# Kernel optimization log

Measured on AMD Instinct MI355X. Metric: run time of the kernel, lower is better.

The kernel has to match this reference:

```python
import jax, jax.numpy as jnp
import numpy as np

B, L, D, H, DK, DV = 2, 2048, 512, 8, 64, 64
EPS_LN = 1e-6


def setup_inputs() -> dict:
    key = jax.random.key(0)
    ks = jax.random.split(key, 14)
    ws = 0.02  # weight init scale
    inp = {}
    for i, n in enumerate(["q_r", "q_i", "k_r", "k_i", "v_r", "v_i"]):
        inp[n] = jax.random.normal(ks[i], (B, L, D), jnp.float32)
    for j, n in enumerate(["wq_r", "wq_i", "wk_r", "wk_i", "wv_r", "wv_i", "fc_r", "fc_i"]):
        inp[n] = jax.random.normal(ks[6 + j], (D, D), jnp.float32) * ws
    # complextorch CVLayerNorm affine: (2,2,D) weight, diag = 1/sqrt(2); complex bias = 0
    c = np.float32(1.0 / np.sqrt(2.0))
    ln_w = jnp.zeros((2, 2, D), jnp.float32).at[0, 0].set(c).at[1, 1].set(c)
    inp["ln_w"] = ln_w
    inp["ln_b_r"] = jnp.zeros((D,), jnp.float32)
    inp["ln_b_i"] = jnp.zeros((D,), jnp.float32)
    return inp


def _cv_layernorm(x, ln_w, ln_b_r, ln_b_i):
    # covariance-whitening complex LayerNorm over last dim (complextorch style)
    xr, xi = jnp.real(x), jnp.imag(x)
    xr = xr - jnp.mean(xr, axis=-1, keepdims=True)
    xi = xi - jnp.mean(xi, axis=-1, keepdims=True)
    vrr = jnp.mean(xr * xr, axis=-1, keepdims=True) + EPS_LN
    vii = jnp.mean(xi * xi, axis=-1, keepdims=True) + EPS_LN
    vri = jnp.mean(xr * xi, axis=-1, keepdims=True)
    s = jnp.sqrt(vrr * vii - vri * vri)
    t = jnp.sqrt(vrr + vii + 2.0 * s)
    inv = 1.0 / (s * t)
    rrr, rii, rri = (vii + s) * inv, (vrr + s) * inv, -vri * inv
    yr = rrr * xr + rri * xi
    yi = rri * xr + rii * xi
    out_r = ln_w[0, 0] * yr + ln_w[0, 1] * yi + ln_b_r
    out_i = ln_w[1, 0] * yr + ln_w[1, 1] * yi + ln_b_i
    return out_r, out_i


def _mha(q_r, q_i, k_r, k_i, v_r, v_i, wq_r, wq_i, wk_r, wk_i, wv_r, wv_i,
         fc_r, fc_i, ln_w, ln_b_r, ln_b_i):
    q = (q_r + 1j * q_i).astype(jnp.complex64)
    k = (k_r + 1j * k_i).astype(jnp.complex64)
    v = (v_r + 1j * v_i).astype(jnp.complex64)
    Wq = (wq_r + 1j * wq_i).astype(jnp.complex64)
    Wk = (wk_r + 1j * wk_i).astype(jnp.complex64)
    Wv = (wv_r + 1j * wv_i).astype(jnp.complex64)
    Wfc = (fc_r + 1j * fc_i).astype(jnp.complex64)
    b, lq = q.shape[0], q.shape[1]
    # complex linear projections (torch Linear: y = x @ W^T), split into heads
    qh = jnp.einsum('bld,ed->ble', q, Wq).reshape(b, lq, H, DK).transpose(0, 2, 1, 3)
    kh = jnp.einsum('bld,ed->ble', k, Wk).reshape(b, -1, H, DK).transpose(0, 2, 1, 3)
    vh = jnp.einsum('bld,ed->ble', v, Wv).reshape(b, -1, H, DV).transpose(0, 2, 1, 3)
    temp = jnp.float32(DK ** 0.5)
    attn = jnp.einsum('bhqd,bhkd->bhqk', qh / temp, kh)  # [B,H,Lq,Lk] complex
    # CVSoftMax: softmax over magnitude, phase preserved
    mag = jnp.abs(attn)
    w = jax.nn.softmax(mag, axis=-1)
    attn = (w * jnp.exp(1j * jnp.angle(attn))).astype(jnp.complex64)
    out = jnp.einsum('bhqk,bhkd->bhqd', attn, vh)
    out = out.transpose(0, 2, 1, 3).reshape(b, lq, H * DV)
    out = jnp.einsum('ble,de->bld', out, Wfc)
    x = out + q  # residual (dropout is identity at p=0 / eval)
    return _cv_layernorm(x, ln_w, ln_b_r, ln_b_i)


def reference(q_r, q_i, k_r, k_i, v_r, v_i, wq_r, wq_i, wk_r, wk_i, wv_r, wv_i,
              fc_r, fc_i, ln_w, ln_b_r, ln_b_i):
    out_r, out_i = _mha(q_r, q_i, k_r, k_i, v_r, v_i, wq_r, wq_i, wk_r, wk_i,
                        wv_r, wv_i, fc_r, fc_i, ln_w, ln_b_r, ln_b_i)
    # stack real/imag so output is a real float32 tensor [B, L, D, 2]
    return jnp.stack([out_r, out_i], axis=-1)
```

## Files before the change

kernel.cpp:

```cpp
#include <hip/hip_runtime.h>
#include <hip/hip_bf16.h>
#include <math.h>

#define NB 2
#define NL 2048
#define ND 512
#define NH 8
#define NDK 64
#define NROW (NB*NL)
#define HEADSZ (NB*NH*NL*NDK)
#define SEG_BIG ((size_t)NROW*ND)
#define SEG_SMALL ((size_t)ND*ND)
#define TOT_W (8*SEG_SMALL)

typedef __attribute__((ext_vector_type(8))) short bf16x8;
typedef __attribute__((ext_vector_type(4))) float f32x4;

__device__ __align__(16) short g_bfw[TOT_W];
__device__ __align__(16) short g_bq_r[HEADSZ], g_bq_i[HEADSZ];
__device__ __align__(16) short g_bk_r[HEADSZ], g_bk_i[HEADSZ];
__device__ __align__(16) short g_bv_r[HEADSZ], g_bv_i[HEADSZ];
__device__ __align__(16) short g_bo_r[SEG_BIG], g_bo_i[SEG_BIG];
__device__ __align__(16) unsigned g_x[SEG_BIG];
__device__ __align__(16) unsigned g_po[(size_t)2*16*NL*NDK];
__device__ float g_pw[(size_t)2*16*NL];

static __device__ __forceinline__ unsigned pack_bf2(float lo, float hi) {
    __hip_bfloat162 h = __float22bfloat162_rn(make_float2(lo, hi));
    unsigned u;
    __builtin_memcpy(&u, &h, 4);
    return u;
}
static __device__ __forceinline__ float bf_lo(unsigned u) {
    const unsigned v = u << 16;
    float f; __builtin_memcpy(&f, &v, 4);
    return f;
}
static __device__ __forceinline__ float bf_hi(unsigned u) {
    const unsigned v = u & 0xFFFF0000u;
    float f; __builtin_memcpy(&f, &v, 4);
    return f;
}
static __device__ __forceinline__ uint4 ld_cvt(const float* p) {
    const float4 a = *(const float4*)p;
    const float4 b = *(const float4*)(p + 4);
    uint4 o;
    o.x = pack_bf2(a.x, a.y); o.y = pack_bf2(a.z, a.w);
    o.z = pack_bf2(b.x, b.y); o.w = pack_bf2(b.z, b.w);
    return o;
}
static __device__ __forceinline__ bf16x8 negbf(bf16x8 v) {
    #pragma unroll
    for (int e = 0; e < 8; ++e) v[e] ^= (short)0x8000;
    return v;
}

struct GPtrs {
    const float* xr[3]; const float* xi[3];
    const float* rr; const float* ri;
};
struct WPtrs { const float* p[8]; };

__global__ __launch_bounds__(256)
void tobf(WPtrs wp)
{
    const size_t i = ((size_t)blockIdx.x*256 + threadIdx.x) * 8;
    if (i >= TOT_W) return;
    const int seg = (int)(i / SEG_SMALL);
    const size_t off = i % SEG_SMALL;
    const uint4 v = ld_cvt(wp.p[seg] + off);
    const int r7 = (int)(off >> 9) & 7;
    const int g  = (int)(off >> 3) & 7;
    const size_t dst = (off & ~(size_t)0x38) | ((size_t)(g ^ r7) << 3);
    *(uint4*)(g_bfw + (size_t)seg*SEG_SMALL + dst) = v;
}

template<int MODE>
__global__ __launch_bounds__(256, 2)
void bgemm(GPtrs gp)
{
    __shared__ __align__(16) short sAB[16384];

    const int bm = blockIdx.x, bn = blockIdx.y;
    const int which = (MODE == 0) ? blockIdx.z : 3;
    const int tx = threadIdx.x;
    const int wave = tx >> 6, lane = tx & 63;
    const int l15 = lane & 15, l4 = lane >> 4;

    const float* Xr = nullptr;
    const float* Xi = nullptr;
    if constexpr (MODE == 0) { Xr = gp.xr[which]; Xi = gp.xi[which]; }
    const short* Wr = g_bfw + (size_t)(2*which)*SEG_SMALL;
    const short* Wi = g_bfw + (size_t)(2*which+1)*SEG_SMALL;

    const int t0r = tx >> 3;
    const int t0g = tx & 7;

    f32x4 Cr[4] = {}, Ci[4] = {};

    for (int kk = 0; kk < ND; kk += 64) {
        uint4 va0, va1, va2, va3;
        if constexpr (MODE == 0) {
            const size_t a0 = (size_t)(bm*64 + t0r)*ND + kk + t0g*8;
            const size_t a1 = a0 + (size_t)32*ND;
            va0 = ld_cvt(Xr + a0); va1 = ld_cvt(Xi + a0);
            va2 = ld_cvt(Xr + a1); va3 = ld_cvt(Xi + a1);
        }
        if constexpr (MODE == 0) {
            #pragma unroll
            for (int i_ = 0; i_ < 4; ++i_) {
                const int within = (i_ & 1)*256 + tx;
                const short* plane = (i_ >> 1) ? Wi : Wr;
                __builtin_amdgcn_global_load_lds(
                    (const __attribute__((address_space(1))) void*)
                        (plane + (size_t)(bn*64 + (within >> 3))*ND + kk + (within & 7)*8),
                    (__attribute__((address_space(3))) void*)
                        &sAB[8192 + (i_ >> 1)*4096 + within*8], 16, 0, 0);
            }
        } else {
            #pragma unroll
            for (int i_ = 0; i_ < 8; ++i_) {
                const int within = (i_ & 1)*256 + tx;
                const int pl = i_ >> 1;
                const short* plane = (pl == 0) ? g_bo_r : (pl == 1) ? g_bo_i : (pl == 2) ? Wr : Wi;
                const int row0 = (pl < 2) ? bm*64 : bn*64;
                __builtin_amdgcn_global_load_lds(
                    (const __attribute__((address_space(1))) void*)
                        (plane + (size_t)(row0 + (within >> 3))*ND + kk + (within & 7)*8),
                    (__attribute__((address_space(3))) void*)
                        &sAB[pl*4096 + within*8], 16, 0, 0);
            }
        }
        if constexpr (MODE == 0) {
            const int g0 = (t0g ^ (t0r & 7)) << 3;
            const int g1 = (t0g ^ ((t0r + 32) & 7)) << 3;
            *(uint4*)&sAB[t0r*64 + g0]               = va0;
            *(uint4*)&sAB[4096 + t0r*64 + g0]        = va1;
            *(uint4*)&sAB[(t0r+32)*64 + g1]          = va2;
            *(uint4*)&sAB[4096 + (t0r+32)*64 + g1]   = va3;
        }
        asm volatile("s_waitcnt vmcnt(0)" ::: "memory");
        __syncthreads();

        #pragma unroll
        for (int ks = 0; ks < 2; ++ks) {
            const int arow = 16*wave + l15;
            const int ag = ((ks*4 + l4) ^ (arow & 7)) << 3;
            const bf16x8 aAr = *(const bf16x8*)&sAB[arow*64 + ag];
            const bf16x8 aAi = *(const bf16x8*)&sAB[4096 + arow*64 + ag];
            const bf16x8 aAn = negbf(aAi);
            #pragma unroll
            for (int nt = 0; nt < 4; ++nt) {
                const int brow = nt*16 + l15;
                const int bg = ((ks*4 + l4) ^ (brow & 7)) << 3;
                const bf16x8 bBr = *(const bf16x8*)&sAB[8192  + brow*64 + bg];
                const bf16x8 bBi = *(const bf16x8*)&sAB[12288 + brow*64 + bg];
                Cr[nt] = __builtin_amdgcn_mfma_f32_16x16x32_bf16(aAr, bBr, Cr[nt], 0, 0, 0);
                Cr[nt] = __builtin_amdgcn_mfma_f32_16x16x32_bf16(aAn, bBi, Cr[nt], 0, 0, 0);
                Ci[nt] = __builtin_amdgcn_mfma_f32_16x16x32_bf16(aAr, bBi, Ci[nt], 0, 0, 0);
                Ci[nt] = __builtin_amdgcn_mfma_f32_16x16x32_bf16(aAi, bBr, Ci[nt], 0, 0, 0);
            }
        }
        __syncthreads();
    }

    const int m0 = bm*64 + 16*wave + 4*l4;
    if constexpr (MODE == 0) {
        if (which == 2) {
            const int bb = m0 >> 11, ll = m0 & (NL-1);
            const int c = ll >> 5, lgrp = (ll >> 3) & 3, e = ll & 7;
            #pragma unroll
            for (int nt = 0; nt < 4; ++nt) {
                const int d = nt*16 + l15;
                const int r = d & 31, dpart = d >> 5;
                const int p = (4*dpart + lgrp) ^ (r & 7);
                const size_t off = (size_t)(bb*NH + bn)*(NL*NDK) + (size_t)c*2048 + (r*8 + p)*8 + e;
                *(uint2*)(g_bv_r + off) = make_uint2(pack_bf2(Cr[nt][0], Cr[nt][1]),
                                                     pack_bf2(Cr[nt][2], Cr[nt][3]));
                *(uint2*)(g_bv_i + off) = make_uint2(pack_bf2(Ci[nt][0], Ci[nt][1]),
                                                     pack_bf2(Ci[nt][2], Ci[nt][3]));
            }
        } else {
            const float s = (which == 0) ? 0.125f : 1.0f;
            short* Pr = (which == 0) ? g_bq_r : g_bk_r;
            short* Pi = (which == 0) ? g_bq_i : g_bk_i;
            #pragma unroll
            for (int r = 0; r < 4; ++r) {
                const int m = m0 + r;
                const int bb = m >> 11, ll = m & (NL-1);
                const size_t base = ((size_t)(bb*NH + bn)*NL + ll)*NDK;
                #pragma unroll
                for (int nt = 0; nt < 4; ++nt) {
                    int col = nt*16 + l15;
                    if (which == 1)
                        col = (col & 7) | ((((col >> 3) ^ (ll & 7))) << 3);
                    const unsigned pk = pack_bf2(Cr[nt][r]*s, Ci[nt][r]*s);
                    Pr[base + col] = (short)(pk & 0xFFFFu);
                    Pi[base + col] = (short)(pk >> 16);
                }
            }
        }
    } else {
        const float* Rr = gp.rr;
        const float* Ri = gp.ri;
        #pragma unroll
        for (int r = 0; r < 4; ++r) {
            const int m = m0 + r;
            const size_t base = (size_t)m*ND + bn*64;
            #pragma unroll
            for (int nt = 0; nt < 4; ++nt) {
                const size_t idx = base + nt*16 + l15;
                g_x[idx] = pack_bf2(Cr[nt][r] + Rr[idx], Ci[nt][r] + Ri[idx]);
            }
        }
    }
}

__global__ __launch_bounds__(256, 4)
void cattn()
{
    __shared__ __align__(16) short sKV[2][8192];
    __shared__ __align__(16) short sCr[64][32], sCi[64][32];

    const int nb = blockIdx.x;
    const int xcd = nb & 7, rest = nb >> 3;
    const int bh = xcd*2 + (rest >> 6);
    const int within = rest & 63;
    const int q0 = (within >> 1) * 64;
    const int half = within & 1;

    const int tx = threadIdx.x;
    const int wave = tx >> 6, lane = tx & 63;
    const int l15 = lane & 15, l4 = lane >> 4;

    const short* Kr = g_bk_r + (size_t)bh*NL*NDK;
    const short* Ki = g_bk_i + (size_t)bh*NL*NDK;
    const short* Vr = g_bv_r + (size_t)bh*NL*NDK;
    const short* Vi = g_bv_i + (size_t)bh*NL*NDK;

    bf16x8 aQr[2], aQi[2], aQn[2];
    {
        const size_t qb = ((size_t)bh*NL + q0 + 16*wave + l15)*NDK + 8*l4;
        aQr[0] = *(const bf16x8*)(g_bq_r + qb);
        aQr[1] = *(const bf16x8*)(g_bq_r + qb + 32);
        aQi[0] = *(const bf16x8*)(g_bq_i + qb);
        aQi[1] = *(const bf16x8*)(g_bq_i + qb + 32);
        aQn[0] = negbf(aQi[0]); aQn[1] = negbf(aQi[1]);
    }

    f32x4 Or[4] = {}, Oi[4] = {};
    float ws[4] = {0.f, 0.f, 0.f, 0.f};

    const short* kvplane = (wave == 0) ? Kr : (wave == 1) ? Ki : (wave == 2) ? Vr : Vi;
    const int pbase = wave * 2048;

    #define STAGE_KV(CHUNK, BUF) do {                                         \
        _Pragma("unroll")                                                     \
        for (int i_ = 0; i_ < 4; ++i_) {                                      \
            const int u_ = i_*64 + lane;                                      \
            __builtin_amdgcn_global_load_lds(                                 \
                (const __attribute__((address_space(1))) void*)               \
                    (kvplane + (size_t)(CHUNK)*2048 + (size_t)u_*8),          \
                (__attribute__((address_space(3))) void*)                     \
                    &sKV[BUF][pbase + u_*8], 16, 0, 0);                       \
        }                                                                     \
    } while (0)

    const int cbase = half * 32;
    STAGE_KV(cbase, 0);
    asm volatile("s_waitcnt vmcnt(0)" ::: "memory");
    __syncthreads();

    const float LOG2E = 1.44269504f;
    const float SHIFT = -4.0f*1.44269504f;

    for (int t = 0; t < 32; ++t) {
        const int cur = t & 1, nxt = cur ^ 1;
        if (t < 31) STAGE_KV(cbase + t + 1, nxt);

        #pragma unroll
        for (int tt = 0; tt < 2; ++tt) {
            const int row = tt*16 + l15;
            const int swb = row & 7;
            f32x4 Sr = {}, Si = {};
            __builtin_amdgcn_s_setprio(1);
            #pragma unroll
            for (int c = 0; c < 2; ++c) {
                const int off = (((c*4 + l4) ^ swb) << 3);
                const bf16x8 bKr = *(const bf16x8*)&sKV[cur][row*64 + off];
                const bf16x8 bKi = *(const bf16x8*)&sKV[cur][2048 + row*64 + off];
                Sr = __builtin_amdgcn_mfma_f32_16x16x32_bf16(aQr[c], bKr, Sr, 0, 0, 0);
                Sr = __builtin_amdgcn_mfma_f32_16x16x32_bf16(aQn[c], bKi, Sr, 0, 0, 0);
                Si = __builtin_amdgcn_mfma_f32_16x16x32_bf16(aQr[c], bKi, Si, 0, 0, 0);
                Si = __builtin_amdgcn_mfma_f32_16x16x32_bf16(aQi[c], bKr, Si, 0, 0, 0);
            }
            __builtin_amdgcn_s_setprio(0);
            const int kgrp = row >> 3;
            #pragma unroll
            for (int r = 0; r < 4; ++r) {
                const int qrow = 16*wave + 4*l4 + r;
                const float s2 = fmaxf(fmaf(Sr[r], Sr[r], Si[r]*Si[r]), 1e-30f);
                const float irs = __builtin_amdgcn_rsqf(s2);
                const float mag = s2 * irs;
                const float w = exp2f(fmaf(mag, LOG2E, SHIFT));
                const float sc = w * irs;
                ws[r] += w;
                const int col = (row & 7) | ((kgrp ^ ((qrow >> 2) & 3)) << 3);
                const unsigned pk = pack_bf2(Sr[r]*sc, Si[r]*sc);
                sCr[qrow][col] = (short)(pk & 0xFFFFu);
                sCi[qrow][col] = (short)(pk >> 16);
            }
        }

        asm volatile("s_waitcnt lgkmcnt(0)" ::: "memory");
        __builtin_amdgcn_sched_barrier(0);

        bf16x8 aCr, aCi, aCn;
        {
            const int qrow = 16*wave + l15;
            const int off = (l4 ^ ((qrow >> 2) & 3)) << 3;
            aCr = *(const bf16x8*)&sCr[qrow][off];
            aCi = *(const bf16x8*)&sCi[qrow][off];
            aCn = negbf(aCi);
        }
        __builtin_amdgcn_s_setprio(1);
        #pragma unroll
        for (int tt = 0; tt < 4; ++tt) {
            const int d = tt*16 + l15;
            const int r = d & 31, dpart = tt >> 1;
            const int p = (4*dpart + l4) ^ (r & 7);
            const int vb = r*64 + p*8;
            const bf16x8 bVr = *(const bf16x8*)&sKV[cur][4096 + vb];
            const bf16x8 bVi = *(const bf16x8*)&sKV[cur][6144 + vb];
            Or[tt] = __builtin_amdgcn_mfma_f32_16x16x32_bf16(aCr, bVr, Or[tt], 0, 0, 0);
            Or[tt] = __builtin_amdgcn_mfma_f32_16x16x32_bf16(aCn, bVi, Or[tt], 0, 0, 0);
            Oi[tt] = __builtin_amdgcn_mfma_f32_16x16x32_bf16(aCr, bVi, Oi[tt], 0, 0, 0);
            Oi[tt] = __builtin_amdgcn_mfma_f32_16x16x32_bf16(aCi, bVr, Oi[tt], 0, 0, 0);
        }
        __builtin_amdgcn_s_setprio(0);

        asm volatile("s_waitcnt vmcnt(0)" ::: "memory");
        __syncthreads();
    }

    #pragma unroll
    for (int r = 0; r < 4; ++r) {
        #pragma unroll
        for (int off = 8; off; off >>= 1) ws[r] += __shfl_xor(ws[r], off);
    }
    const size_t pb = (size_t)(half*16 + bh)*NL;
    if (l15 == 0) {
        #pragma unroll
        for (int r = 0; r < 4; ++r)
            g_pw[pb + q0 + 16*wave + 4*l4 + r] = ws[r];
    }
    #pragma unroll
    for (int tt = 0; tt < 4; ++tt) {
        const int d = tt*16 + l15;
        #pragma unroll
        for (int r = 0; r < 4; ++r) {
            const int q = q0 + 16*wave + 4*l4 + r;
            g_po[(pb + q)*NDK + d] = pack_bf2(Or[tt][r], Oi[tt][r]);
        }
    }
    #undef STAGE_KV
}

__global__ __launch_bounds__(256)
void comb()
{
    const size_t t4 = ((size_t)blockIdx.x*256 + threadIdx.x) * 4;
    const int d = (int)(t4 & 63);
    const int q = (int)((t4 >> 6) & (NL-1));
    const int bh = (int)(t4 >> 17);
    const size_t p = ((size_t)bh*NL + q)*NDK + d;
    const uint4 a = *(const uint4*)&g_po[p];
    const uint4 c = *(const uint4*)&g_po[(size_t)16*NL*NDK + p];
    const float w = g_pw[(size_t)bh*NL + q] + g_pw[(size_t)(16 + bh)*NL + q];
    const float inv = 1.0f / w;
    float fr[4], fi[4];
    fr[0] = (bf_lo(a.x) + bf_lo(c.x))*inv; fi[0] = (bf_hi(a.x) + bf_hi(c.x))*inv;
    fr[1] = (bf_lo(a.y) + bf_lo(c.y))*inv; fi[1] = (bf_hi(a.y) + bf_hi(c.y))*inv;
    fr[2] = (bf_lo(a.z) + bf_lo(c.z))*inv; fi[2] = (bf_hi(a.z) + bf_hi(c.z))*inv;
    fr[3] = (bf_lo(a.w) + bf_lo(c.w))*inv; fi[3] = (bf_hi(a.w) + bf_hi(c.w))*inv;
    const int b = bh >> 3, h = bh & 7;
    const int dsw = ((((d >> 3) ^ (q & 7))) << 3) | (d & 7);
    const size_t o = ((size_t)b*NL + q)*ND + h*NDK + dsw;
    *(uint2*)(g_bo_r + o) = make_uint2(pack_bf2(fr[0], fr[1]), pack_bf2(fr[2], fr[3]));
    *(uint2*)(g_bo_i + o) = make_uint2(pack_bf2(fi[0], fi[1]), pack_bf2(fi[2], fi[3]));
}

__global__ __launch_bounds__(256)
void cvln(const float* __restrict__ ln_w, const float* __restrict__ lnb_r,
          const float* __restrict__ lnb_i, float2* __restrict__ out)
{
    __shared__ float red[4][5];
    const int row = blockIdx.x, tx = threadIdx.x;
    const unsigned* xp = g_x + (size_t)row*ND;
    const unsigned u0 = xp[tx], u1 = xp[tx + 256];
    const float a0 = bf_lo(u0), a1 = bf_lo(u1);
    const float b0 = bf_hi(u0), b1 = bf_hi(u1);
    float s_r = a0 + a1, s_i = b0 + b1;
    float srr = a0*a0 + a1*a1, sii = b0*b0 + b1*b1, sri = a0*b0 + a1*b1;
    #pragma unroll
    for (int off = 32; off; off >>= 1) {
        s_r += __shfl_xor(s_r, off);  s_i += __shfl_xor(s_i, off);
        srr += __shfl_xor(srr, off);  sii += __shfl_xor(sii, off);
        sri += __shfl_xor(sri, off);
    }
    const int wave = tx >> 6, lane = tx & 63;
    if (lane == 0) { red[wave][0]=s_r; red[wave][1]=s_i; red[wave][2]=srr; red[wave][3]=sii; red[wave][4]=sri; }
    __syncthreads();
    s_r = red[0][0]+red[1][0]+red[2][0]+red[3][0];
    s_i = red[0][1]+red[1][1]+red[2][1]+red[3][1];
    srr = red[0][2]+red[1][2]+red[2][2]+red[3][2];
    sii = red[0][3]+red[1][3]+red[2][3]+red[3][3];
    sri = red[0][4]+red[1][4]+red[2][4]+red[3][4];

    const float invD = 1.0f/ND;
    const float mr = s_r*invD, mi = s_i*invD;
    const float vrr = srr*invD - mr*mr + 1e-6f;
    const float vii = sii*invD - mi*mi + 1e-6f;
    const float vri = sri*invD - mr*mi;
    const float s  = sqrtf(vrr*vii - vri*vri);
    const float t  = sqrtf(vrr + vii + 2.0f*s);
    const float inv = 1.0f/(s*t);
    const float rrr = (vii + s)*inv, rii = (vrr + s)*inv, rri = -vri*inv;

    #pragma unroll
    for (int p = 0; p < 2; ++p) {
        const int d = tx + p*256;
        const float cxr = (p ? a1 : a0) - mr;
        const float cxi = (p ? b1 : b0) - mi;
        const float yr = rrr*cxr + rri*cxi;
        const float yi = rri*cxr + rii*cxi;
        const float w00 = ln_w[d], w01 = ln_w[512 + d];
        const float w10 = ln_w[1024 + d], w11 = ln_w[1536 + d];
        out[(size_t)row*ND + d] = make_float2(w00*yr + w01*yi + lnb_r[d],
                                              w10*yr + w11*yi + lnb_i[d]);
    }
}

extern "C" void kernel_launch(void* const* d_in, const int* in_sizes, int n_in,
                              void* d_out, int out_size, void* d_ws, size_t ws_size,
                              hipStream_t stream)
{
    (void)in_sizes; (void)n_in; (void)d_ws; (void)ws_size; (void)out_size;
    const float* ln_w = (const float*)d_in[14];
    const float* lnbr = (const float*)d_in[15];
    const float* lnbi = (const float*)d_in[16];

    GPtrs gp;
    gp.xr[0] = (const float*)d_in[0];  gp.xi[0] = (const float*)d_in[1];
    gp.xr[1] = (const float*)d_in[2];  gp.xi[1] = (const float*)d_in[3];
    gp.xr[2] = (const float*)d_in[4];  gp.xi[2] = (const float*)d_in[5];
    gp.rr = (const float*)d_in[0];     gp.ri = (const float*)d_in[1];

    WPtrs wp;
    for (int j = 0; j < 8; ++j) wp.p[j] = (const float*)d_in[6 + j];

    const int wcvt_blocks = (int)((TOT_W/8 + 255)/256);
    tobf<<<wcvt_blocks, 256, 0, stream>>>(wp);
    bgemm<0><<<dim3(NROW/64, ND/64, 3), 256, 0, stream>>>(gp);
    cattn<<<1024, 256, 0, stream>>>();
    comb<<<2048, 256, 0, stream>>>();
    bgemm<1><<<dim3(NROW/64, ND/64), 256, 0, stream>>>(gp);
    cvln<<<NROW, 256, 0, stream>>>(ln_w, lnbr, lnbi, (float2*)d_out);
}
```

Measured before the change: 162.4 us.

## Quad-buffer K/V staging, two chunks per barrier, fold log2e into Q scale

The attention kernel's K/V shared-memory staging grows from a double to a quad buffer. The loop now processes two chunks per iteration, prefetching two chunks ahead and synchronising once per pair, which halves the block-wide barriers. V fragments are loaded from LDS before the wait so their latency overlaps the softmax work, and their swizzled offsets are precomputed. The log2(e) factor is folded into the Q scaling, which removes an FMA per score. The price is doubling sKV to 64 KB, which may cut the number of resident blocks per CU below the launch-bounds target of 4 and so reduce latency hiding.

```diff
diff --git a/kernel.cpp b/kernel.cpp
--- a/kernel.cpp
+++ b/kernel.cpp
@@ -181,7 +181,7 @@
                                                      pack_bf2(Ci[nt][2], Ci[nt][3]));
             }
         } else {
-            const float s = (which == 0) ? 0.125f : 1.0f;
+            const float s = (which == 0) ? 0.18033688f : 1.0f;
             short* Pr = (which == 0) ? g_bq_r : g_bk_r;
             short* Pi = (which == 0) ? g_bq_i : g_bk_i;
             #pragma unroll
@@ -219,7 +219,7 @@
 __global__ __launch_bounds__(256, 4)
 void cattn()
 {
-    __shared__ __align__(16) short sKV[2][8192];
+    __shared__ __align__(16) short sKV[4][8192];
     __shared__ __align__(16) short sCr[64][32], sCi[64][32];
 
     const int nb = blockIdx.x;
@@ -266,79 +266,99 @@
         }                                                                     \
     } while (0)
 
+    const float SHIFT = -5.770780163f;
+
+    int voff[4];
+    #pragma unroll
+    for (int tt = 0; tt < 4; ++tt) {
+        const int r = (tt*16 + l15) & 31, dpart = tt >> 1;
+        const int p = (4*dpart + l4) ^ (r & 7);
+        voff[tt] = r*64 + p*8;
+    }
+
+    #define CHUNK_COMPUTE(BUF) do {                                           \
+        _Pragma("unroll")                                                     \
+        for (int tt = 0; tt < 2; ++tt) {                                      \
+            const int row = tt*16 + l15;                                      \
+            const int swb = row & 7;                                          \
+            f32x4 Sr = {}, Si = {};                                           \
+            __builtin_amdgcn_s_setprio(1);                                    \
+            _Pragma("unroll")                                                 \
+            for (int c = 0; c < 2; ++c) {                                     \
+                const int off = (((c*4 + l4) ^ swb) << 3);                    \
+                const bf16x8 bKr = *(const bf16x8*)&sKV[BUF][row*64 + off];   \
+                const bf16x8 bKi = *(const bf16x8*)&sKV[BUF][2048 + row*64 + off]; \
+                Sr = __builtin_amdgcn_mfma_f32_16x16x32_bf16(aQr[c], bKr, Sr, 0, 0, 0); \
+                Sr = __builtin_amdgcn_mfma_f32_16x16x32_bf16(aQn[c], bKi, Sr, 0, 0, 0); \
+                Si = __builtin_amdgcn_mfma_f32_16x16x32_bf16(aQr[c], bKi, Si, 0, 0, 0); \
+                Si = __builtin_amdgcn_mfma_f32_16x16x32_bf16(aQi[c], bKr, Si, 0, 0, 0); \
+            }                                                                 \
+            __builtin_amdgcn_s_setprio(0);                                    \
+            const int kgrp = row >> 3;                                        \
+            _Pragma("unroll")                                                 \
+            for (int r = 0; r < 4; ++r) {                                     \
+                const int qrow = 16*wave + 4*l4 + r;                          \
+                const float s2 = fmaxf(fmaf(Sr[r], Sr[r], Si[r]*Si[r]), 1e-30f); \
+                const float irs = __builtin_amdgcn_rsqf(s2);                  \
+                const float mag = s2 * irs;                                   \
+                const float w = exp2f(mag + SHIFT);                           \
+                const float sc = w * irs;                                     \
+                ws[r] += w;                                                   \
+                const int col = (row & 7) | ((kgrp ^ ((qrow >> 2) & 3)) << 3); \
+                const unsigned pk = pack_bf2(Sr[r]*sc, Si[r]*sc);             \
+                sCr[qrow][col] = (short)(pk & 0xFFFFu);                       \
+                sCi[qrow][col] = (short)(pk >> 16);                           \
+            }                                                                 \
+        }                                                                     \
+        bf16x8 vfr0 = *(const bf16x8*)&sKV[BUF][4096 + voff[0]];              \
+        bf16x8 vfi0 = *(const bf16x8*)&sKV[BUF][6144 + voff[0]];              \
+        bf16x8 vfr1 = *(const bf16x8*)&sKV[BUF][4096 + voff[1]];              \
+        bf16x8 vfi1 = *(const bf16x8*)&sKV[BUF][6144 + voff[1]];              \
+        bf16x8 vfr2 = *(const bf16x8*)&sKV[BUF][4096 + voff[2]];              \
+        bf16x8 vfi2 = *(const bf16x8*)&sKV[BUF][6144 + voff[2]];              \
+        bf16x8 vfr3 = *(const bf16x8*)&sKV[BUF][4096 + voff[3]];              \
+        bf16x8 vfi3 = *(const bf16x8*)&sKV[BUF][6144 + voff[3]];              \
+        asm volatile("s_waitcnt lgkmcnt(0)" ::: "memory");                    \
+        __builtin_amdgcn_sched_barrier(0);                                    \
+        bf16x8 aCr, aCi, aCn;                                                 \
+        {                                                                     \
+            const int qrow = 16*wave + l15;                                   \
+            const int off = (l4 ^ ((qrow >> 2) & 3)) << 3;                    \
+            aCr = *(const bf16x8*)&sCr[qrow][off];                            \
+            aCi = *(const bf16x8*)&sCi[qrow][off];                            \
+            aCn = negbf(aCi);                                                 \
+        }                                                                     \
+        __builtin_amdgcn_s_setprio(1);                                        \
+        Or[0] = __builtin_amdgcn_mfma_f32_16x16x32_bf16(aCr, vfr0, Or[0], 0, 0, 0); \
+        Or[0] = __builtin_amdgcn_mfma_f32_16x16x32_bf16(aCn, vfi0, Or[0], 0, 0, 0); \
+        Oi[0] = __builtin_amdgcn_mfma_f32_16x16x32_bf16(aCr, vfi0, Oi[0], 0, 0, 0); \
+        Oi[0] = __builtin_amdgcn_mfma_f32_16x16x32_bf16(aCi, vfr0, Oi[0], 0, 0, 0); \
+        Or[1] = __builtin_amdgcn_mfma_f32_16x16x32_bf16(aCr, vfr1, Or[1], 0, 0, 0); \
+        Or[1] = __builtin_amdgcn_mfma_f32_16x16x32_bf16(aCn, vfi1, Or[1], 0, 0, 0); \
+        Oi[1] = __builtin_amdgcn_mfma_f32_16x16x32_bf16(aCr, vfi1, Oi[1], 0, 0, 0); \
+        Oi[1] = __builtin_amdgcn_mfma_f32_16x16x32_bf16(aCi, vfr1, Oi[1], 0, 0, 0); \
+        Or[2] = __builtin_amdgcn_mfma_f32_16x16x32_bf16(aCr, vfr2, Or[2], 0, 0, 0); \
+        Or[2] = __builtin_amdgcn_mfma_f32_16x16x32_bf16(aCn, vfi2, Or[2], 0, 0, 0); \
+        Oi[2] = __builtin_amdgcn_mfma_f32_16x16x32_bf16(aCr, vfi2, Oi[2], 0, 0, 0); \
+        Oi[2] = __builtin_amdgcn_mfma_f32_16x16x32_bf16(aCi, vfr2, Oi[2], 0, 0, 0); \
+        Or[3] = __builtin_amdgcn_mfma_f32_16x16x32_bf16(aCr, vfr3, Or[3], 0, 0, 0); \
+        Or[3] = __builtin_amdgcn_mfma_f32_16x16x32_bf16(aCn, vfi3, Or[3], 0, 0, 0); \
+        Oi[3] = __builtin_amdgcn_mfma_f32_16x16x32_bf16(aCr, vfi3, Oi[3], 0, 0, 0); \
+        Oi[3] = __builtin_amdgcn_mfma_f32_16x16x32_bf16(aCi, vfr3, Oi[3], 0, 0, 0); \
+        __builtin_amdgcn_s_setprio(0);                                        \
+    } while (0)
+
     const int cbase = half * 32;
-    STAGE_KV(cbase, 0);
+    STAGE_KV(cbase + 0, 0);
+    STAGE_KV(cbase + 1, 1);
     asm volatile("s_waitcnt vmcnt(0)" ::: "memory");
     __syncthreads();
 
-    const float LOG2E = 1.44269504f;
-    const float SHIFT = -4.0f*1.44269504f;
-
-    for (int t = 0; t < 32; ++t) {
-        const int cur = t & 1, nxt = cur ^ 1;
-        if (t < 31) STAGE_KV(cbase + t + 1, nxt);
-
-        #pragma unroll
-        for (int tt = 0; tt < 2; ++tt) {
-            const int row = tt*16 + l15;
-            const int swb = row & 7;
-            f32x4 Sr = {}, Si = {};
-            __builtin_amdgcn_s_setprio(1);
-            #pragma unroll
-            for (int c = 0; c < 2; ++c) {
-                const int off = (((c*4 + l4) ^ swb) << 3);
-                const bf16x8 bKr = *(const bf16x8*)&sKV[cur][row*64 + off];
-                const bf16x8 bKi = *(const bf16x8*)&sKV[cur][2048 + row*64 + off];
-                Sr = __builtin_amdgcn_mfma_f32_16x16x32_bf16(aQr[c], bKr, Sr, 0, 0, 0);
-                Sr = __builtin_amdgcn_mfma_f32_16x16x32_bf16(aQn[c], bKi, Sr, 0, 0, 0);
-                Si = __builtin_amdgcn_mfma_f32_16x16x32_bf16(aQr[c], bKi, Si, 0, 0, 0);
-                Si = __builtin_amdgcn_mfma_f32_16x16x32_bf16(aQi[c], bKr, Si, 0, 0, 0);
-            }
-            __builtin_amdgcn_s_setprio(0);
-            const int kgrp = row >> 3;
-            #pragma unroll
-            for (int r = 0; r < 4; ++r) {
-                const int qrow = 16*wave + 4*l4 + r;
-                const float s2 = fmaxf(fmaf(Sr[r], Sr[r], Si[r]*Si[r]), 1e-30f);
-                const float irs = __builtin_amdgcn_rsqf(s2);
-                const float mag = s2 * irs;
-                const float w = exp2f(fmaf(mag, LOG2E, SHIFT));
-                const float sc = w * irs;
-                ws[r] += w;
-                const int col = (row & 7) | ((kgrp ^ ((qrow >> 2) & 3)) << 3);
-                const unsigned pk = pack_bf2(Sr[r]*sc, Si[r]*sc);
-                sCr[qrow][col] = (short)(pk & 0xFFFFu);
-                sCi[qrow][col] = (short)(pk >> 16);
-            }
-        }
-
-        asm volatile("s_waitcnt lgkmcnt(0)" ::: "memory");
-        __builtin_amdgcn_sched_barrier(0);
-
-        bf16x8 aCr, aCi, aCn;
-        {
-            const int qrow = 16*wave + l15;
-            const int off = (l4 ^ ((qrow >> 2) & 3)) << 3;
-            aCr = *(const bf16x8*)&sCr[qrow][off];
-            aCi = *(const bf16x8*)&sCi[qrow][off];
-            aCn = negbf(aCi);
-        }
-        __builtin_amdgcn_s_setprio(1);
-        #pragma unroll
-        for (int tt = 0; tt < 4; ++tt) {
-            const int d = tt*16 + l15;
-            const int r = d & 31, dpart = tt >> 1;
-            const int p = (4*dpart + l4) ^ (r & 7);
-            const int vb = r*64 + p*8;
-            const bf16x8 bVr = *(const bf16x8*)&sKV[cur][4096 + vb];
-            const bf16x8 bVi = *(const bf16x8*)&sKV[cur][6144 + vb];
-            Or[tt] = __builtin_amdgcn_mfma_f32_16x16x32_bf16(aCr, bVr, Or[tt], 0, 0, 0);
-            Or[tt] = __builtin_amdgcn_mfma_f32_16x16x32_bf16(aCn, bVi, Or[tt], 0, 0, 0);
-            Oi[tt] = __builtin_amdgcn_mfma_f32_16x16x32_bf16(aCr, bVi, Oi[tt], 0, 0, 0);
-            Oi[tt] = __builtin_amdgcn_mfma_f32_16x16x32_bf16(aCi, bVr, Oi[tt], 0, 0, 0);
-        }
-        __builtin_amdgcn_s_setprio(0);
-
+    for (int t = 0; t < 32; t += 2) {
+        if (t + 2 < 32) STAGE_KV(cbase + t + 2, (t + 2) & 3);
+        if (t + 3 < 32) STAGE_KV(cbase + t + 3, (t + 3) & 3);
+        CHUNK_COMPUTE(t & 3);
+        CHUNK_COMPUTE((t + 1) & 3);
         asm volatile("s_waitcnt vmcnt(0)" ::: "memory");
         __syncthreads();
     }
@@ -363,6 +383,7 @@
             g_po[(pb + q)*NDK + d] = pack_bf2(Or[tt][r], Oi[tt][r]);
         }
     }
+    #undef CHUNK_COMPUTE
     #undef STAGE_KV
 }
 
```

New measurement: 172.4 us. 1.06x slower.
